# Kernel optimization log

Measured on AMD Instinct MI355X. Metric: run time of the kernel, lower is better.

Reference implementation:

```python
import jax, jax.numpy as jnp
import numpy as np

N, B, E, D, DQ, H = 20000, 32, 320000, 128, 1024, 2
L = N // B  # 625 nodes per graph (equal-size graphs -> static max_node_num)
NUM_GNN_LAYERS = 3


def setup_inputs() -> dict:
    key = jax.random.key(0)
    ks = jax.random.split(key, 32)
    rn = lambda k, s, scale=1.0: jax.random.normal(k, s, jnp.float32) * scale
    w = lambda k, fi, fo: rn(k, (fi, fo), 1.0 / np.sqrt(fi))
    inp = {
        'x': rn(ks[0], (N, D)),
        'edge_attr': rn(ks[1], (E, D)),
        'u': rn(ks[2], (B, D)),
        'qa_attr': rn(ks[3], (B, DQ)),
        # edge MLP: cat(src,dest,edge_attr,u[eb]) = 4D -> hidden D -> D
        'W_e1': w(ks[4], 4 * D, D), 'b_e1': jnp.zeros((D,)),
        'W_e2': w(ks[5], D, D), 'b_e2': jnp.zeros((D,)),
        # weight mlp: cat(edge_attr, u[eb]) = 2D -> 1 (num_layers=1)
        'W_w': w(ks[6], 2 * D, 1), 'b_w': jnp.zeros((1,)),
        # message mlp: cat(x[row], edge_attr) = 2D -> D -> D
        'W_m1': w(ks[7], 2 * D, D), 'b_m1': jnp.zeros((D,)),
        'W_m2': w(ks[8], D, D), 'b_m2': jnp.zeros((D,)),
        # update mlp: cat(x, received, u[nb]) = 3D -> D -> D
        'W_u1': w(ks[9], 3 * D, D), 'b_u1': jnp.zeros((D,)),
        'W_u2': w(ks[10], D, D), 'b_u2': jnp.zeros((D,)),
        # multihead att-pool: q from qa_attr (DQ) -> H*dk; k,v from evidence (D) -> H*dk
        'W_q': w(ks[11], DQ, D), 'b_q': jnp.zeros((D,)),
        'W_k': w(ks[12], D, D), 'b_k': jnp.zeros((D,)),
        'W_v': w(ks[13], D, D), 'b_v': jnp.zeros((D,)),
        'edge_index': jax.random.randint(ks[14], (2, E), 0, N, dtype=jnp.int32),
        'node_batch': (jnp.arange(N, dtype=jnp.int32) // L).astype(jnp.int32),
        'num_of_nodes': jnp.full((B,), L, dtype=jnp.int32),
    }
    return inp


def _mlp2(h, W1, b1, W2, b2):
    return jax.nn.relu(h @ W1 + b1) @ W2 + b2


def _seg_softmax(logits, seg, num):
    m = jax.ops.segment_max(logits, seg, num_segments=num)
    e = jnp.exp(logits - m[seg])
    s = jax.ops.segment_sum(e, seg, num_segments=num)
    return e / s[seg]


def reference(x, edge_attr, u, qa_attr,
              W_e1, b_e1, W_e2, b_e2, W_w, b_w,
              W_m1, b_m1, W_m2, b_m2, W_u1, b_u1, W_u2, b_u2,
              W_q, b_q, W_k, b_k, W_v, b_v,
              edge_index, node_batch, num_of_nodes):
    row, col = edge_index[0], edge_index[1]
    edge_batch = node_batch[row]
    Bsz, Nn = u.shape[0], x.shape[0]
    Lm = Nn // Bsz  # static max_node_num (equal-size graphs)

    norm_w = None
    for _ in range(NUM_GNN_LAYERS):
        ue = u[edge_batch]  # [E, D]
        # EdgeModel: cat(src, dest, edge_attr, u[eb]) -> MLP -> new edge_attr
        new_edge = _mlp2(jnp.concatenate([x[row], x[col], edge_attr, ue], 1),
                         W_e1, b_e1, W_e2, b_e2)
        # edge weights from OLD edge_attr (per EdgeV1Model.forward)
        wts = jnp.concatenate([edge_attr, ue], 1) @ W_w + b_w  # [E,1]
        norm_w = _seg_softmax(wts[:, 0], edge_batch, Bsz)[:, None]  # [E,1]
        edge_attr = new_edge
        # NodeModel: message MLP, weighted scatter_mean over col, update MLP
        msg = _mlp2(jnp.concatenate([x[row], edge_attr], 1), W_m1, b_m1, W_m2, b_m2)
        summed = jax.ops.segment_sum(msg * norm_w, col, num_segments=Nn)
        cnt = jax.ops.segment_sum(jnp.ones((msg.shape[0],), msg.dtype), col, num_segments=Nn)
        received = summed / jnp.maximum(cnt, 1.0)[:, None]
        x = _mlp2(jnp.concatenate([x, received, u[node_batch]], 1),
                  W_u1, b_u1, W_u2, b_u2)

    pooled_edge = jax.ops.segment_sum(edge_attr * norm_w, edge_batch, num_segments=Bsz)  # [B,D]
    # evidence packing: equal graphs -> simple reshape, then exact GELU
    evidence = jax.nn.gelu(x.reshape(Bsz, Lm, -1), approximate=False)  # [B,L,D]
    mask = jnp.arange(Lm)[None, :] >= num_of_nodes[:, None]  # [B,L] True = masked

    # MultiheadAttPoolLayer
    dk = W_k.shape[1] // H
    q = (qa_attr @ W_q + b_q).reshape(Bsz, H, dk)
    k = (evidence @ W_k + b_k).reshape(Bsz, Lm, H, dk)
    v = (evidence @ W_v + b_v).reshape(Bsz, Lm, H, dk)
    scores = jnp.einsum('bhd,blhd->bhl', q, k) / jnp.sqrt(jnp.float32(dk))
    scores = jnp.where(mask[:, None, :], -1e30, scores)
    attn = jax.nn.softmax(scores, axis=-1)
    pooled_node = jnp.einsum('bhl,blhd->bhd', attn, v).reshape(Bsz, H * dk)  # [B,D]

    return jnp.concatenate([pooled_edge, pooled_node], 1)  # [B, 2D]
```

## Files before the change

kernel.cpp:

```cpp
#include <hip/hip_runtime.h>
#include <math.h>

typedef __bf16 bf16_t;
typedef bf16_t bf16x8 __attribute__((ext_vector_type(8)));
typedef bf16_t bf16x4 __attribute__((ext_vector_type(4)));
typedef bf16_t bf16x2 __attribute__((ext_vector_type(2)));
typedef float  f32x4  __attribute__((ext_vector_type(4)));

#define N_NODES 20000
#define NEDGE   320000
#define DIM     128
#define TP      136
#define EBLK    2500
#define FWAVES  10000
#define NBLK    625
#define GPRE    157
#define PBLK    512

#define FE1  0
#define FE2  49152
#define FM1  65536
#define FM2  98304
#define FU1  114688
#define FU2  163840
#define FK   180224
#define FV   196608
#define FWC  212992
#define WF_ELEMS 229376

__device__ __forceinline__ void acc_zero32(f32x4 acc[2][8]) {
  f32x4 z = {0.f, 0.f, 0.f, 0.f};
#pragma unroll
  for (int i = 0; i < 2; ++i)
#pragma unroll
    for (int j = 0; j < 8; ++j) acc[i][j] = z;
}

__device__ __forceinline__ void wstage_rows_bf(bf16_t* sA, const bf16_t* src, int rowreg, int lane) {
  int r = lane >> 1, h = lane & 1;
  int row = __shfl(rowreg, r);
  const bf16_t* sp = src + (size_t)row * DIM + h * 64;
  bf16_t* dp = sA + r * TP + h * 64;
#pragma unroll
  for (int i = 0; i < 8; ++i)
    *(uint4*)(dp + i * 8) = *(const uint4*)(sp + i * 8);
}

__device__ __forceinline__ void wstage_rows_f32(bf16_t* sA, const float* src, int rowreg, int lane) {
  int r = lane >> 1, h = lane & 1;
  int row = __shfl(rowreg, r);
  const float* sp = src + (size_t)row * DIM + h * 64;
  bf16_t* dp = sA + r * TP + h * 64;
#pragma unroll
  for (int i = 0; i < 8; ++i) {
    float4 f0 = *(const float4*)(sp + i * 8);
    float4 f1 = *(const float4*)(sp + i * 8 + 4);
    bf16x8 tv;
    tv[0]=(bf16_t)f0.x; tv[1]=(bf16_t)f0.y; tv[2]=(bf16_t)f0.z; tv[3]=(bf16_t)f0.w;
    tv[4]=(bf16_t)f1.x; tv[5]=(bf16_t)f1.y; tv[6]=(bf16_t)f1.z; tv[7]=(bf16_t)f1.w;
    *(bf16x8*)(dp + i * 8) = tv;
  }
}

__device__ __forceinline__ void wstage_seq_bf(bf16_t* sA, const bf16_t* src, int base, int lane) {
  int r = lane >> 1, h = lane & 1;
  const bf16_t* sp = src + (size_t)(base + r) * DIM + h * 64;
  bf16_t* dp = sA + r * TP + h * 64;
#pragma unroll
  for (int i = 0; i < 8; ++i)
    *(uint4*)(dp + i * 8) = *(const uint4*)(sp + i * 8);
}

__device__ __forceinline__ void wstage_seq_f32(bf16_t* sA, const float* src, int base, int lane) {
  int r = lane >> 1, h = lane & 1;
  const float* sp = src + (size_t)(base + r) * DIM + h * 64;
  bf16_t* dp = sA + r * TP + h * 64;
#pragma unroll
  for (int i = 0; i < 8; ++i) {
    float4 f0 = *(const float4*)(sp + i * 8);
    float4 f1 = *(const float4*)(sp + i * 8 + 4);
    bf16x8 tv;
    tv[0]=(bf16_t)f0.x; tv[1]=(bf16_t)f0.y; tv[2]=(bf16_t)f0.z; tv[3]=(bf16_t)f0.w;
    tv[4]=(bf16_t)f1.x; tv[5]=(bf16_t)f1.y; tv[6]=(bf16_t)f1.z; tv[7]=(bf16_t)f1.w;
    *(bf16x8*)(dp + i * 8) = tv;
  }
}

__device__ __forceinline__ void chunk_stage(bf16_t* ch, const bf16_t* __restrict__ src, int t) {
#pragma unroll
  for (int i = 0; i < 8; ++i) {
    int idx = (i * 256 + t) * 8;
    *(uint4*)(ch + idx) = *(const uint4*)(src + idx);
  }
}

__device__ __forceinline__ void wmfma_lds(const bf16_t* sA, const bf16_t* ch,
                                          int lane, int lm, int lq, f32x4 acc[2][8]) {
#pragma unroll
  for (int kk = 0; kk < 4; ++kk) {
    int ko = kk * 32 + lq * 8;
    bf16x8 a0 = *(const bf16x8*)(sA + lm * TP + ko);
    bf16x8 a1 = *(const bf16x8*)(sA + (16 + lm) * TP + ko);
    const bf16_t* wp = ch + (kk << 12) + (lane << 3);
#pragma unroll
    for (int ct = 0; ct < 8; ++ct) {
      bf16x8 bfr = *(const bf16x8*)(wp + (ct << 9));
      acc[0][ct] = __builtin_amdgcn_mfma_f32_16x16x32_bf16(a0, bfr, acc[0][ct], 0, 0, 0);
      acc[1][ct] = __builtin_amdgcn_mfma_f32_16x16x32_bf16(a1, bfr, acc[1][ct], 0, 0, 0);
    }
  }
}

__device__ __forceinline__ void wmfma_gk128(const bf16_t* sA, const bf16_t* __restrict__ Wf,
                                            int lane, int lm, int lq, f32x4 acc[2][8]) {
#pragma unroll
  for (int kk = 0; kk < 4; ++kk) {
    int ko = kk * 32 + lq * 8;
    bf16x8 a0 = *(const bf16x8*)(sA + lm * TP + ko);
    bf16x8 a1 = *(const bf16x8*)(sA + (16 + lm) * TP + ko);
    const bf16_t* wp = Wf + ((kk * 8) << 9) + (lane << 3);
#pragma unroll
    for (int ct = 0; ct < 8; ++ct) {
      bf16x8 bfr = *(const bf16x8*)(wp + (ct << 9));
      acc[0][ct] = __builtin_amdgcn_mfma_f32_16x16x32_bf16(a0, bfr, acc[0][ct], 0, 0, 0);
      acc[1][ct] = __builtin_amdgcn_mfma_f32_16x16x32_bf16(a1, bfr, acc[1][ct], 0, 0, 0);
    }
  }
}

__device__ __forceinline__ void merge_shfl(float& m, float& s, int width) {
  for (int k = 1; k < width; k <<= 1) {
    float m2 = __shfl_xor(m, k), s2 = __shfl_xor(s, k);
    float M = fmaxf(m, m2), ns = 0.f;
    if (m  > -1e29f) ns += s  * expf(m  - M);
    if (m2 > -1e29f) ns += s2 * expf(m2 - M);
    m = M; s = ns;
  }
}

__global__ void gn_xcvt(const float* x, bf16_t* xb) {
  int i = blockIdx.x * 256 + threadIdx.x;
  if (i < N_NODES * DIM / 4) {
    float4 f = ((const float4*)x)[i];
    bf16x4 o; o[0]=(bf16_t)f.x; o[1]=(bf16_t)f.y; o[2]=(bf16_t)f.z; o[3]=(bf16_t)f.w;
    *(bf16x4*)(xb + (size_t)i * 4) = o;
  }
}

__global__ void gn_wcomb(const float* Wm2, const float* Wu1, float* wc) {
  int idx = blockIdx.x * 256 + threadIdx.x;
  if (idx >= 16384) return;
  int i = idx >> 7, j = idx & 127;
  float acc = 0.f;
  for (int m = 0; m < 128; ++m)
    acc += Wm2[i * 128 + m] * Wu1[(128 + m) * 128 + j];
  wc[idx] = acc;
}

__global__ void gn_fragw(const float* We1, const float* We2, const float* Wm1, const float* Wm2,
                         const float* Wu1, const float* Wu2, const float* Wk, const float* Wv,
                         const float* Wc, bf16_t* WF) {
  int idx = blockIdx.x * 256 + threadIdx.x;
  if (idx >= WF_ELEMS) return;
  int seg = idx >> 14;
  const float* W; int kc;
  switch (seg) {
    case 0:  W = We1; kc = 0; break;
    case 1:  W = We1; kc = 1; break;
    case 2:  W = We1; kc = 2; break;
    case 3:  W = We2; kc = 0; break;
    case 4:  W = Wm1; kc = 0; break;
    case 5:  W = Wm1; kc = 1; break;
    case 6:  W = Wm2; kc = 0; break;
    case 7:  W = Wu1; kc = 0; break;
    case 8:  W = Wu1; kc = 1; break;
    case 9:  W = Wu1; kc = 2; break;
    case 10: W = Wu2; kc = 0; break;
    case 11: W = Wk;  kc = 0; break;
    case 12: W = Wv;  kc = 0; break;
    default: W = Wc;  kc = 0; break;
  }
  int r = idx & 16383;
  int j = r & 7, lane = (r >> 3) & 63, ct = (r >> 9) & 7, kk = (r >> 12) & 3;
  int k = kc * 128 + kk * 32 + (lane >> 4) * 8 + j;
  int n = ct * 16 + (lane & 15);
  WF[idx] = (bf16_t)W[k * 128 + n];
}

__global__ void gn_uprep(const float* u, const float* We1, const float* be1,
                         const float* Ww, const float* bw,
                         const float* bm2, const float* Wu1,
                         float* Rp, float* uw, float* bm2u) {
  int t = threadIdx.x;
  for (int idx = blockIdx.x * 256 + t; idx < 32 * 128; idx += gridDim.x * 256) {
    int g = idx >> 7, c = idx & 127;
    float acc = be1[c];
    for (int k = 0; k < 128; ++k) acc += u[g * 128 + k] * We1[(384 + k) * 128 + c];
    Rp[g * 128 + (c & 15) * 8 + (c >> 4)] = acc;
  }
  if (blockIdx.x == 0 && t < 32) {
    float acc = bw[0];
    for (int k = 0; k < 128; ++k) acc += u[t * 128 + k] * Ww[128 + k];
    uw[t] = acc;
  }
  if (blockIdx.x == 1 && t < 128) {
    float acc = 0.f;
    for (int k = 0; k < 128; ++k) acc += bm2[k] * Wu1[(128 + k) * 128 + t];
    bm2u[t] = acc;
  }
}

__global__ void gn_counti(const int* ei, int* cnti) {
  int e = blockIdx.x * 256 + threadIdx.x;
  if (e < NEDGE) atomicAdd(&cnti[ei[NEDGE + e]], 1);
}

__global__ void gn_scan(const int* cnti, int* off, int* curs) {
  __shared__ int part[256];
  int t = threadIdx.x;
  int base = t * 80;
  int lim = base + 80; if (lim > N_NODES) lim = N_NODES;
  int s = 0;
  for (int i = base; i < lim; ++i) s += cnti[i];
  part[t] = s;
  __syncthreads();
  for (int d = 1; d < 256; d <<= 1) {
    int add = (t >= d) ? part[t - d] : 0;
    __syncthreads();
    part[t] += add;
    __syncthreads();
  }
  int pfx = (t == 0) ? 0 : part[t - 1];
  for (int i = base; i < lim; ++i) {
    off[i] = pfx; curs[i] = pfx; pfx += cnti[i];
  }
  if (t == 0) off[N_NODES] = NEDGE;
}

__global__ void gn_eidx(const int* ei, int* curs, int* eidx) {
  int e = blockIdx.x * 256 + threadIdx.x;
  if (e < NEDGE) {
    int c = ei[NEDGE + e];
    int pos = atomicAdd(&curs[c], 1);
    eidx[pos] = e;
  }
}

__global__ void gn_q(const float* qa, const float* Wq, const float* bq, float* qb) {
  int b = blockIdx.x, t = threadIdx.x;
  int c = t & 127, half = t >> 7;
  const float* qrow = qa + b * 1024 + half * 512;
  float acc = 0.f;
  for (int k = 0; k < 512; ++k) acc += qrow[k] * Wq[(half * 512 + k) * 128 + c];
  __shared__ float red[256];
  red[t] = acc;
  __syncthreads();
  if (half == 0) qb[b * 128 + c] = red[c] + red[128 + c] + bq[c];
}

__global__ void gn_wl0(const float* ea, const float* Ww, const float* uw,
                       const int* ei, const int* nbat, float* wl, int* gb) {
  int t = threadIdx.x;
  int sub = t & 15, grp = t >> 4;
  for (int e = blockIdx.x * 16 + grp; e < NEDGE; e += gridDim.x * 16) {
    const float* er = ea + (size_t)e * DIM + sub * 8;
    float s = 0.f;
#pragma unroll
    for (int j = 0; j < 8; ++j) s += er[j] * Ww[sub * 8 + j];
#pragma unroll
    for (int m = 1; m < 16; m <<= 1) s += __shfl_xor(s, m);
    if (sub == 0) {
      int g = nbat[ei[e]];
      wl[e] = s + uw[g];
      gb[e] = g;
    }
  }
}

__global__ void gn_part0(const float* wl, const int* gb, float* pm, float* ps) {
  __shared__ float lv[128];
  __shared__ int   lgg[128];
  int t = threadIdx.x, blk = blockIdx.x, e0 = blk * 128;
  if (t < 128) { lv[t] = wl[e0 + t]; lgg[t] = gb[e0 + t]; }
  __syncthreads();
  int g = t >> 3, seg = t & 7;
  float m = -1e30f, s = 0.f;
  for (int i = seg * 16; i < seg * 16 + 16; ++i)
    if (lgg[i] == g) {
      float v = lv[i];
      if (v > m) { s = s * expf(m - v) + 1.f; m = v; }
      else s += expf(v - m);
    }
  merge_shfl(m, s, 8);
  if (seg == 0) { pm[g * FWAVES + blk] = m; ps[g * FWAVES + blk] = s; }
}

__global__ void gn_reduce_ms(const float* pm, const float* ps, float* mg, float* sg, int nb) {
  int g = blockIdx.x, t = threadIdx.x;
  __shared__ float red[256];
  float m = -1e30f;
  for (int i = t; i < nb; i += 256) m = fmaxf(m, pm[g * FWAVES + i]);
  red[t] = m; __syncthreads();
  for (int s2 = 128; s2 > 0; s2 >>= 1) { if (t < s2) red[t] = fmaxf(red[t], red[t + s2]); __syncthreads(); }
  m = red[0]; __syncthreads();
  float s = 0.f;
  for (int i = t; i < nb; i += 256) {
    float sb = ps[g * FWAVES + i];
    if (sb > 0.f) s += sb * expf(pm[g * FWAVES + i] - m);
  }
  red[t] = s; __syncthreads();
  for (int s2 = 128; s2 > 0; s2 >>= 1) { if (t < s2) red[t] += red[t + s2]; __syncthreads(); }
  if (t == 0) { mg[g] = m; sg[g] = red[0]; }
}

__global__ __launch_bounds__(256, 2) void gn_fused(
    const bf16_t* __restrict__ xb,
    const void* esrcv, int efirst,
    bf16_t* edst,
    const bf16_t* __restrict__ WF,
    const float* Rp, const float* UW, const float* Wwv,
    const float* be2, const float* bm1,
    const float* wl_cur, const float* mg, const float* sg,
    float* wl_next, float* pm, float* ps, int last,
    const int* ei, const int* gb, bf16_t* msg,
    const float* uu, const float* bu1, const int* nbat, float* pre,
    float* nwout) {
  __shared__ bf16_t chunk[16384];
  __shared__ bf16_t band[4][32 * TP];
  __shared__ float slwt[128];

  int t = threadIdx.x;
  int w = t >> 6, lane = t & 63;
  int lm = lane & 15, lq = lane >> 4;
  int blk = blockIdx.x;
  bf16_t* myband = band[w];

  if (blk >= EBLK) {
    int nb128 = blk - EBLK;
    int gb32 = nb128 * 4 + w;
    int lrow = 0, lgr = 0;
    if (lane < 32) {
      int node = gb32 * 32 + lane;
      if (node > N_NODES - 1) node = N_NODES - 1;
      lrow = node;
      lgr = nbat[node];
    }
    f32x4 acc[2][8];
    acc_zero32(acc);
    wstage_rows_bf(myband, xb, lrow, lane);
    chunk_stage(chunk, WF + FU1, t);
    __syncthreads();
    wmfma_lds(myband, chunk, lane, lm, lq, acc);
    __syncthreads();
    wstage_rows_f32(myband, uu, lgr, lane);
    chunk_stage(chunk, WF + FU1 + 32768, t);
    __syncthreads();
    wmfma_lds(myband, chunk, lane, lm, lq, acc);
    if (gb32 < NBLK) {
      float* pp = pre + (size_t)gb32 * 4096 + lane;
#pragma unroll
      for (int rt = 0; rt < 2; ++rt)
#pragma unroll
        for (int reg = 0; reg < 4; ++reg)
#pragma unroll
          for (int ct = 0; ct < 8; ++ct)
            pp[((rt * 32 + reg * 8 + ct) << 6)] = acc[rt][ct][reg] + bu1[ct * 16 + lm];
    }
    return;
  }

  int e0 = blk * 128;
  int ew0 = e0 + w * 32;
  int lrowr = 0, lcolr = 0, lgr = 0;
  float lnwr = 0.f;
  if (lane < 32) {
    int e = ew0 + lane;
    lrowr = ei[e];
    lcolr = ei[NEDGE + e];
    lgr = gb[e];
    lnwr = expf(wl_cur[e] - mg[lgr]) / sg[lgr];
    nwout[e] = lnwr;
  }

  f32x4 accE[2][8], accM[2][8];
  acc_zero32(accE);
  acc_zero32(accM);

  uint4 c0, c1, c2, c3, c4, c5, c6, c7;
#define CLOAD(SRC) { const uint4* _s = (const uint4*)(SRC) + t; \
  c0 = _s[0];    c1 = _s[256];  c2 = _s[512];  c3 = _s[768]; \
  c4 = _s[1024]; c5 = _s[1280]; c6 = _s[1536]; c7 = _s[1792]; }
#define CWRITE() { uint4* _d = (uint4*)chunk + t; \
  _d[0] = c0;    _d[256] = c1;  _d[512] = c2;  _d[768] = c3; \
  _d[1024] = c4; _d[1280] = c5; _d[1536] = c6; _d[1792] = c7; }

  CLOAD(WF + FE1);
  wstage_rows_bf(myband, xb, lrowr, lane);
  CWRITE();
  __syncthreads();

  CLOAD(WF + FM1);
  wmfma_lds(myband, chunk, lane, lm, lq, accE);
  __syncthreads();
  CWRITE();
  __syncthreads();

  CLOAD(WF + FE1 + 16384);
  wmfma_lds(myband, chunk, lane, lm, lq, accM);
  wstage_rows_bf(myband, xb, lcolr, lane);
  __syncthreads();
  CWRITE();
  __syncthreads();

  CLOAD(WF + FE1 + 32768);
  wmfma_lds(myband, chunk, lane, lm, lq, accE);
  if (efirst) wstage_seq_f32(myband, (const float*)esrcv, ew0, lane);
  else        wstage_seq_bf (myband, (const bf16_t*)esrcv, ew0, lane);
  __syncthreads();
  CWRITE();
  __syncthreads();

  CLOAD(WF + FE2);
  wmfma_lds(myband, chunk, lane, lm, lq, accE);
#pragma unroll
  for (int rt = 0; rt < 2; ++rt)
#pragma unroll
    for (int reg = 0; reg < 4; ++reg) {
      int row = rt * 16 + lq * 4 + reg;
      int g = __shfl(lgr, row);
      const float4* rp = (const float4*)(Rp + (size_t)g * 128 + lm * 8);
      float4 ra = rp[0], rb = rp[1];
      float rv[8] = {ra.x, ra.y, ra.z, ra.w, rb.x, rb.y, rb.z, rb.w};
#pragma unroll
      for (int ct = 0; ct < 8; ++ct) {
        int col = ct * 16 + lm;
        myband[row * TP + col] = (bf16_t)fmaxf(accE[rt][ct][reg] + rv[ct], 0.f);
      }
    }
  acc_zero32(accE);
  __syncthreads();
  CWRITE();
  __syncthreads();

  CLOAD(WF + FM1 + 16384);
  wmfma_lds(myband, chunk, lane, lm, lq, accE);
  {
    float ww8[8], be8[8];
#pragma unroll
    for (int ct = 0; ct < 8; ++ct) { ww8[ct] = Wwv[ct * 16 + lm]; be8[ct] = be2[ct * 16 + lm]; }
#pragma unroll
    for (int rt = 0; rt < 2; ++rt)
#pragma unroll
      for (int reg = 0; reg < 4; ++reg) {
        int row = rt * 16 + lq * 4 + reg;
        int g = __shfl(lgr, row);
        float lsum = 0.f;
#pragma unroll
        for (int ct = 0; ct < 8; ++ct) {
          int col = ct * 16 + lm;
          float v = accE[rt][ct][reg] + be8[ct];
          myband[row * TP + col] = (bf16_t)v;
          lsum += v * ww8[ct];
        }
        if (!last) {
          lsum += __shfl_xor(lsum, 1);
          lsum += __shfl_xor(lsum, 2);
          lsum += __shfl_xor(lsum, 4);
          lsum += __shfl_xor(lsum, 8);
          if (lm == 0) {
            float v2 = lsum + UW[g];
            wl_next[ew0 + row] = v2;
            slwt[w * 32 + row] = v2;
          }
        }
      }
    int r = lane >> 1, h = lane & 1;
    bf16_t* dp = edst + (size_t)(ew0 + r) * DIM + h * 64;
    const bf16_t* sp2 = myband + r * TP + h * 64;
#pragma unroll
    for (int i = 0; i < 8; ++i)
      *(uint4*)(dp + i * 8) = *(const uint4*)(sp2 + i * 8);
  }
  __syncthreads();
  CWRITE();
  __syncthreads();

  wmfma_lds(myband, chunk, lane, lm, lq, accM);
  {
    float bm18[8];
#pragma unroll
    for (int ct = 0; ct < 8; ++ct) bm18[ct] = bm1[ct * 16 + lm];
#pragma unroll
    for (int rt = 0; rt < 2; ++rt)
#pragma unroll
      for (int reg = 0; reg < 4; ++reg) {
        int row = rt * 16 + lq * 4 + reg;
        float nwv = __shfl(lnwr, row);
#pragma unroll
        for (int ct = 0; ct < 8; ++ct) {
          int col = ct * 16 + lm;
          myband[row * TP + col] = (bf16_t)(fmaxf(accM[rt][ct][reg] + bm18[ct], 0.f) * nwv);
        }
      }
    int r = lane >> 1, h = lane & 1;
    bf16_t* dp = msg + (size_t)(ew0 + r) * DIM + h * 64;
    const bf16_t* sp2 = myband + r * TP + h * 64;
#pragma unroll
    for (int i = 0; i < 8; ++i)
      *(uint4*)(dp + i * 8) = *(const uint4*)(sp2 + i * 8);
  }

  if (!last) {
    int g = lane >> 1, seg = lane & 1;
    float m = -1e30f, s = 0.f;
    for (int i = seg * 16; i < seg * 16 + 16; ++i) {
      int gi = __shfl(lgr, i);
      if (gi == g) {
        float v = slwt[w * 32 + i];
        if (v > m) { s = s * expf(m - v) + 1.f; m = v; }
        else s += expf(v - m);
      }
    }
    merge_shfl(m, s, 2);
    if (seg == 0) { pm[g * FWAVES + blk * 4 + w] = m; ps[g * FWAVES + blk * 4 + w] = s; }
  }
#undef CLOAD
#undef CWRITE
}

__global__ __launch_bounds__(256) void gn_gather(
    const bf16_t* __restrict__ msg, const float* __restrict__ nw,
    const int* __restrict__ off, const int* __restrict__ eidx,
    bf16_t* recvb, float* rnw) {
  int w = threadIdx.x >> 6, lane = threadIdx.x & 63;
  int n = blockIdx.x * 4 + w;
  int o0 = off[n], o1 = off[n + 1];
  float a0 = 0.f, a1 = 0.f, snw = 0.f;
  int i = o0;
  int e = (i < o1) ? eidx[i] : 0;
  for (; i < o1; ++i) {
    int en = (i + 1 < o1) ? eidx[i + 1] : 0;
    bf16x2 v = *(const bf16x2*)(msg + (size_t)e * DIM + lane * 2);
    a0 += (float)v[0];
    a1 += (float)v[1];
    snw += nw[e];
    e = en;
  }
  float ic = 1.f / fmaxf((float)(o1 - o0), 1.f);
  bf16x2 o; o[0] = (bf16_t)(a0 * ic); o[1] = (bf16_t)(a1 * ic);
  *(bf16x2*)(recvb + (size_t)n * DIM + lane * 2) = o;
  if (lane == 0) rnw[n] = snw * ic;
}

__global__ __launch_bounds__(64, 3) void gn_node(
    bf16_t* xdst, const bf16_t* recvb, const float* rnw, const float* pre,
    const bf16_t* __restrict__ WF, const float* bu2, const float* bm2u) {
  __shared__ bf16_t sA[32 * TP];

  int lane = threadIdx.x;
  int nb = blockIdx.x;
  int n0 = nb * 32;
  int lm = lane & 15, lq = lane >> 4;

  float rnwreg = 0.f;
  if (lane < 32) rnwreg = rnw[n0 + lane];

  wstage_seq_bf(sA, recvb, n0, lane);

  f32x4 acc[2][8];
  acc_zero32(acc);
  wmfma_gk128(sA, WF + FWC, lane, lm, lq, acc);

  const float* pp = pre + (size_t)nb * 4096 + lane;
  float bm2u8[8];
#pragma unroll
  for (int ct = 0; ct < 8; ++ct) bm2u8[ct] = bm2u[ct * 16 + lm];
#pragma unroll
  for (int rt = 0; rt < 2; ++rt)
#pragma unroll
    for (int reg = 0; reg < 4; ++reg) {
      int row = rt * 16 + lq * 4 + reg;
      float rv = __shfl(rnwreg, row);
#pragma unroll
      for (int ct = 0; ct < 8; ++ct) {
        int col = ct * 16 + lm;
        sA[row * TP + col] = (bf16_t)fmaxf(
            acc[rt][ct][reg] + rv * bm2u8[ct] + pp[((rt * 32 + reg * 8 + ct) << 6)], 0.f);
      }
    }
  acc_zero32(acc);
  wmfma_gk128(sA, WF + FU2, lane, lm, lq, acc);

  {
    float bu28[8];
#pragma unroll
    for (int ct = 0; ct < 8; ++ct) bu28[ct] = bu2[ct * 16 + lm];
#pragma unroll
    for (int rt = 0; rt < 2; ++rt)
#pragma unroll
      for (int reg = 0; reg < 4; ++reg) {
        int row = rt * 16 + lq * 4 + reg;
        bf16_t* dr = xdst + (size_t)(n0 + row) * DIM;
#pragma unroll
        for (int ct = 0; ct < 8; ++ct) {
          int col = ct * 16 + lm;
          dr[col] = (bf16_t)(acc[rt][ct][reg] + bu28[ct]);
        }
      }
  }
}

__global__ __launch_bounds__(64, 3) void gn_ev(
    const bf16_t* xsrc, const bf16_t* __restrict__ WF,
    const float* bk, const float* bv, float* kb, float* vb) {
  __shared__ bf16_t sA[32 * TP];

  int lane = threadIdx.x;
  int n0 = blockIdx.x * 32;
  int sel = blockIdx.y;
  const bf16_t* Wf = WF + (sel ? FV : FK);
  const float* bias = sel ? bv : bk;
  float* dst = sel ? vb : kb;
  int lm = lane & 15, lq = lane >> 4;

  {
    int r = lane >> 1, h = lane & 1;
    const bf16_t* sp = xsrc + (size_t)(n0 + r) * DIM + h * 64;
    bf16_t* dp = sA + r * TP + h * 64;
#pragma unroll
    for (int i = 0; i < 8; ++i) {
      uint4 v = *(const uint4*)(sp + i * 8);
      bf16_t tmp[8];
      *(uint4*)tmp = v;
      bf16x8 tv;
#pragma unroll
      for (int j = 0; j < 8; ++j) {
        float f = (float)tmp[j];
        tv[j] = (bf16_t)(0.5f * f * (1.f + erff(f * 0.70710678118654752f)));
      }
      *(bf16x8*)(dp + i * 8) = tv;
    }
  }

  f32x4 acc[2][8];
  acc_zero32(acc);
  wmfma_gk128(sA, Wf, lane, lm, lq, acc);

  {
    float b8[8];
#pragma unroll
    for (int ct = 0; ct < 8; ++ct) b8[ct] = bias[ct * 16 + lm];
#pragma unroll
    for (int rt = 0; rt < 2; ++rt)
#pragma unroll
      for (int reg = 0; reg < 4; ++reg) {
        int row = rt * 16 + lq * 4 + reg;
        float* dr = dst + (size_t)(n0 + row) * DIM;
#pragma unroll
        for (int ct = 0; ct < 8; ++ct) {
          int col = ct * 16 + lm;
          dr[col] = acc[rt][ct][reg] + b8[ct];
        }
      }
  }
}

__global__ __launch_bounds__(256, 2) void gn_pooled_edge(
    const bf16_t* __restrict__ eb, const float* __restrict__ nw,
    const int* __restrict__ gb, float* pep) {
  __shared__ float loc[4][4096];
  int t = threadIdx.x;
  int lane = t & 63, w = t >> 6;
  float* myloc = loc[w];
  for (int i = lane; i < 4096; i += 64) myloc[i] = 0.f;

  int wid = blockIdx.x * 4 + w;
  int c0 = lane * 2;
  for (int e = wid; e < NEDGE; e += PBLK * 4) {
    int g = gb[e];
    float nwt = nw[e];
    bf16x2 v = *(const bf16x2*)(eb + (size_t)e * DIM + c0);
    float* a = myloc + g * 128 + c0;
    float2 cur = *(float2*)a;
    cur.x += (float)v[0] * nwt;
    cur.y += (float)v[1] * nwt;
    *(float2*)a = cur;
  }
  __syncthreads();
  float* pp = pep + (size_t)blockIdx.x * 4096;
  for (int i = t; i < 4096; i += 256)
    pp[i] = loc[0][i] + loc[1][i] + loc[2][i] + loc[3][i];
}

__global__ void gn_att(const float* qb, const float* kb, const float* vb, const int* non, float* out) {
  int b = blockIdx.x >> 1, h = blockIdx.x & 1, t = threadIdx.x;
  __shared__ float qv[64];
  __shared__ float sc[625];
  __shared__ float red[256];
  if (t < 64) qv[t] = qb[b * 128 + h * 64 + t];
  __syncthreads();
  int nn = non[b];
  const float4* qv4 = (const float4*)qv;
  for (int l = t; l < 625; l += 256) {
    float acc = 0.f;
    const float4* kr = (const float4*)(kb + ((size_t)(b * 625 + l)) * DIM + h * 64);
#pragma unroll
    for (int d2 = 0; d2 < 16; ++d2) {
      float4 kv = kr[d2];
      float4 qq = qv4[d2];
      acc += qq.x * kv.x + qq.y * kv.y + qq.z * kv.z + qq.w * kv.w;
    }
    sc[l] = (l < nn) ? acc * 0.125f : -1e30f;
  }
  __syncthreads();
  float m = -1e30f;
  for (int l = t; l < 625; l += 256) m = fmaxf(m, sc[l]);
  red[t] = m; __syncthreads();
  for (int s2 = 128; s2 > 0; s2 >>= 1) { if (t < s2) red[t] = fmaxf(red[t], red[t + s2]); __syncthreads(); }
  m = red[0]; __syncthreads();
  float ssum = 0.f;
  for (int l = t; l < 625; l += 256) { float e = expf(sc[l] - m); sc[l] = e; ssum += e; }
  red[t] = ssum; __syncthreads();
  for (int s2 = 128; s2 > 0; s2 >>= 1) { if (t < s2) red[t] += red[t + s2]; __syncthreads(); }
  float inv = 1.f / red[0];
  __syncthreads();
  int d = t & 63, seg = t >> 6;
  float acc = 0.f;
  for (int l = seg; l < 625; l += 4) acc += sc[l] * vb[((size_t)(b * 625 + l)) * DIM + h * 64 + d];
  red[t] = acc; __syncthreads();
  if (t < 64) {
    float v = red[t] + red[64 + t] + red[128 + t] + red[192 + t];
    out[b * 256 + 128 + h * 64 + d] = v * inv;
  }
}

__global__ void gn_fin(const float* pep, float* out) {
  int i = blockIdx.x * 256 + threadIdx.x;
  float s = 0.f;
#pragma unroll 8
  for (int blk = 0; blk < PBLK; ++blk) s += pep[(size_t)blk * 4096 + i];
  int b = i >> 7, c = i & 127;
  out[b * 256 + c] = s;
}

extern "C" void kernel_launch(void* const* d_in, const int* in_sizes, int n_in,
                              void* d_out, int out_size, void* d_ws, size_t ws_size,
                              hipStream_t stream) {
  const float* x   = (const float*)d_in[0];
  const float* ea  = (const float*)d_in[1];
  const float* u   = (const float*)d_in[2];
  const float* qa  = (const float*)d_in[3];
  const float* We1 = (const float*)d_in[4];
  const float* be1 = (const float*)d_in[5];
  const float* We2 = (const float*)d_in[6];
  const float* be2 = (const float*)d_in[7];
  const float* Ww  = (const float*)d_in[8];
  const float* bw  = (const float*)d_in[9];
  const float* Wm1 = (const float*)d_in[10];
  const float* bm1 = (const float*)d_in[11];
  const float* Wm2 = (const float*)d_in[12];
  const float* bm2 = (const float*)d_in[13];
  const float* Wu1 = (const float*)d_in[14];
  const float* bu1 = (const float*)d_in[15];
  const float* Wu2 = (const float*)d_in[16];
  const float* bu2 = (const float*)d_in[17];
  const float* Wq  = (const float*)d_in[18];
  const float* bq  = (const float*)d_in[19];
  const float* Wk  = (const float*)d_in[20];
  const float* bk  = (const float*)d_in[21];
  const float* Wv  = (const float*)d_in[22];
  const float* bv  = (const float*)d_in[23];
  const int* ei   = (const int*)d_in[24];
  const int* nbat = (const int*)d_in[25];
  const int* non  = (const int*)d_in[26];
  float* out = (float*)d_out;

  char* p = (char*)d_ws;
  auto alloc = [&](size_t bytes) { char* r = p; p += (bytes + 255) & ~(size_t)255; return r; };
  bf16_t* EB    = (bf16_t*)alloc((size_t)NEDGE * DIM * 2);
  bf16_t* XB    = (bf16_t*)alloc((size_t)N_NODES * DIM * 2);
  bf16_t* XB0   = (bf16_t*)alloc((size_t)N_NODES * DIM * 2);
  bf16_t* MSG   = (bf16_t*)alloc((size_t)NEDGE * DIM * 2);
  bf16_t* RECVB = (bf16_t*)alloc((size_t)N_NODES * DIM * 2);
  int*   CNTI = (int*)alloc((size_t)N_NODES * 4);
  int*   OFF  = (int*)alloc((size_t)(N_NODES + 1) * 4);
  int*   CURS = (int*)alloc((size_t)N_NODES * 4);
  int*   EIDX = (int*)alloc((size_t)NEDGE * 4);
  float* WL   = (float*)alloc((size_t)NEDGE * 4);
  float* WLn  = (float*)alloc((size_t)NEDGE * 4);
  float* NW   = (float*)alloc((size_t)NEDGE * 4);
  float* RNW  = (float*)alloc((size_t)N_NODES * 4);
  int*   GB   = (int*)alloc((size_t)NEDGE * 4);
  float* PM   = (float*)alloc((size_t)32 * FWAVES * 4);
  float* PS   = (float*)alloc((size_t)32 * FWAVES * 4);
  float* MG   = (float*)alloc(32 * 4);
  float* SG   = (float*)alloc(32 * 4);
  float* RP   = (float*)alloc(32 * 128 * 4);
  float* UW   = (float*)alloc(32 * 4);
  float* WCOMB= (float*)alloc(16384 * 4);
  float* BM2U = (float*)alloc(128 * 4);
  bf16_t* WF  = (bf16_t*)alloc((size_t)WF_ELEMS * 2);
  float* QB   = (float*)alloc(32 * 128 * 4);
  float* KB   = (float*)alloc((size_t)N_NODES * DIM * 4);
  float* VB   = (float*)alloc((size_t)N_NODES * DIM * 4);
  float* PEP  = (float*)alloc((size_t)PBLK * 4096 * 4);
  float* PRE  = (float*)alloc((size_t)N_NODES * DIM * 4);

  hipMemsetAsync(CNTI, 0, (size_t)N_NODES * 4, stream);

  gn_xcvt<<<(N_NODES * DIM / 4 + 255) / 256, 256, 0, stream>>>(x, XB0);
  gn_wcomb<<<64, 256, 0, stream>>>(Wm2, Wu1, WCOMB);
  gn_fragw<<<(WF_ELEMS + 255) / 256, 256, 0, stream>>>(We1, We2, Wm1, Wm2, Wu1, Wu2, Wk, Wv, WCOMB, WF);
  gn_uprep<<<16, 256, 0, stream>>>(u, We1, be1, Ww, bw, bm2, Wu1, RP, UW, BM2U);
  gn_counti<<<1250, 256, 0, stream>>>(ei, CNTI);
  gn_scan<<<1, 256, 0, stream>>>(CNTI, OFF, CURS);
  gn_eidx<<<1250, 256, 0, stream>>>(ei, CURS, EIDX);
  gn_q<<<32, 256, 0, stream>>>(qa, Wq, bq, QB);
  gn_wl0<<<2500, 256, 0, stream>>>(ea, Ww, UW, ei, nbat, WL, GB);
  gn_part0<<<EBLK, 256, 0, stream>>>(WL, GB, PM, PS);

  for (int layer = 0; layer < 3; ++layer) {
    int first = (layer == 0) ? 1 : 0;
    int last = (layer == 2) ? 1 : 0;
    const bf16_t* xs = first ? XB0 : XB;
    const void* es = first ? (const void*)ea : (const void*)EB;
    float* cur = (layer == 1) ? WLn : WL;
    float* nxt = (layer == 1) ? WL : WLn;
    gn_reduce_ms<<<32, 256, 0, stream>>>(PM, PS, MG, SG, first ? EBLK : FWAVES);
    gn_fused<<<EBLK + GPRE, 256, 0, stream>>>(xs, es, first, EB, WF, RP, UW, Ww,
                                              be2, bm1, cur, MG, SG,
                                              nxt, PM, PS, last, ei, GB, MSG,
                                              u, bu1, nbat, PRE, NW);
    gn_gather<<<5000, 256, 0, stream>>>(MSG, NW, OFF, EIDX, RECVB, RNW);
    gn_node<<<NBLK, 64, 0, stream>>>(XB, RECVB, RNW, PRE, WF, bu2, BM2U);
  }

  gn_pooled_edge<<<PBLK, 256, 0, stream>>>(EB, NW, GB, PEP);
  gn_ev<<<dim3(NBLK, 2), 64, 0, stream>>>(XB, WF, bk, bv, KB, VB);
  gn_att<<<64, 256, 0, stream>>>(QB, KB, VB, non, out);
  gn_fin<<<16, 256, 0, stream>>>(PEP, out);
}
```

Baseline: 1.320 ms.

## Fold edge second layer into downstream weights, store pre-projection edge hidden state

The edge MLP's second linear layer (We2) is composed algebraically into its consumers: We1's edge-attr slice, Wm1's edge slice, and the weight-logit vector. Each fused edge block therefore runs one fewer 128x128 MFMA stage and stores the ReLU hidden state instead of the projected edge_attr. The pooled-edge output now applies We2 and a per-graph bias term after the weighted segment sum, which needs an extra small kernel. The gather loop is unrolled by four for more memory-level parallelism, and attention pooling uses 1024 threads per block. Composing weights in bf16 changes rounding slightly.

```diff
diff --git a/kernel.cpp b/kernel.cpp
--- a/kernel.cpp
+++ b/kernel.cpp
@@ -18,9 +18,9 @@
 #define PBLK    512
 
 #define FE1  0
-#define FE2  49152
+#define FCE  49152
 #define FM1  65536
-#define FM2  98304
+#define FCM  81920
 #define FU1  114688
 #define FU2  163840
 #define FK   180224
@@ -147,19 +147,28 @@
   }
 }
 
-__global__ void gn_wcomb(const float* Wm2, const float* Wu1, float* wc) {
+__global__ void gn_wcomb(const float* Wm2, const float* Wu1, const float* We2,
+                         const float* We1, const float* Wm1,
+                         float* wc1, float* wce, float* wcm) {
   int idx = blockIdx.x * 256 + threadIdx.x;
   if (idx >= 16384) return;
   int i = idx >> 7, j = idx & 127;
   float acc = 0.f;
-  for (int m = 0; m < 128; ++m)
-    acc += Wm2[i * 128 + m] * Wu1[(128 + m) * 128 + j];
-  wc[idx] = acc;
-}
-
-__global__ void gn_fragw(const float* We1, const float* We2, const float* Wm1, const float* Wm2,
-                         const float* Wu1, const float* Wu2, const float* Wk, const float* Wv,
-                         const float* Wc, bf16_t* WF) {
+  if (blockIdx.y == 0) {
+    for (int m = 0; m < 128; ++m) acc += Wm2[i * 128 + m] * Wu1[(128 + m) * 128 + j];
+    wc1[idx] = acc;
+  } else if (blockIdx.y == 1) {
+    for (int m = 0; m < 128; ++m) acc += We2[i * 128 + m] * We1[(256 + m) * 128 + j];
+    wce[idx] = acc;
+  } else {
+    for (int m = 0; m < 128; ++m) acc += We2[i * 128 + m] * Wm1[(128 + m) * 128 + j];
+    wcm[idx] = acc;
+  }
+}
+
+__global__ void gn_fragw(const float* We1, const float* Wce, const float* Wm1, const float* Wcm,
+                         const float* Wm2, const float* Wu1, const float* Wu2,
+                         const float* Wk, const float* Wv, const float* Wc1, bf16_t* WF) {
   int idx = blockIdx.x * 256 + threadIdx.x;
   if (idx >= WF_ELEMS) return;
   int seg = idx >> 14;
@@ -168,9 +177,9 @@
     case 0:  W = We1; kc = 0; break;
     case 1:  W = We1; kc = 1; break;
     case 2:  W = We1; kc = 2; break;
-    case 3:  W = We2; kc = 0; break;
+    case 3:  W = Wce; kc = 0; break;
     case 4:  W = Wm1; kc = 0; break;
-    case 5:  W = Wm1; kc = 1; break;
+    case 5:  W = Wcm; kc = 0; break;
     case 6:  W = Wm2; kc = 0; break;
     case 7:  W = Wu1; kc = 0; break;
     case 8:  W = Wu1; kc = 1; break;
@@ -178,7 +187,7 @@
     case 10: W = Wu2; kc = 0; break;
     case 11: W = Wk;  kc = 0; break;
     case 12: W = Wv;  kc = 0; break;
-    default: W = Wc;  kc = 0; break;
+    default: W = Wc1; kc = 0; break;
   }
   int r = idx & 16383;
   int j = r & 7, lane = (r >> 3) & 63, ct = (r >> 9) & 7, kk = (r >> 12) & 3;
@@ -190,23 +199,39 @@
 __global__ void gn_uprep(const float* u, const float* We1, const float* be1,
                          const float* Ww, const float* bw,
                          const float* bm2, const float* Wu1,
-                         float* Rp, float* uw, float* bm2u) {
+                         const float* bm1, const float* be2,
+                         const float* Wm1, const float* We2,
+                         float* Rp0, float* Rp12, float* uw, float* uw2,
+                         float* bm2u, float* bm1p, float* wv) {
   int t = threadIdx.x;
   for (int idx = blockIdx.x * 256 + t; idx < 32 * 128; idx += gridDim.x * 256) {
     int g = idx >> 7, c = idx & 127;
     float acc = be1[c];
     for (int k = 0; k < 128; ++k) acc += u[g * 128 + k] * We1[(384 + k) * 128 + c];
-    Rp[g * 128 + (c & 15) * 8 + (c >> 4)] = acc;
+    float be12 = 0.f;
+    for (int k = 0; k < 128; ++k) be12 += be2[k] * We1[(256 + k) * 128 + c];
+    int tc = g * 128 + (c & 15) * 8 + (c >> 4);
+    Rp0[tc] = acc;
+    Rp12[tc] = acc + be12;
   }
   if (blockIdx.x == 0 && t < 32) {
     float acc = bw[0];
     for (int k = 0; k < 128; ++k) acc += u[t * 128 + k] * Ww[128 + k];
+    float bsh = 0.f;
+    for (int c = 0; c < 128; ++c) bsh += be2[c] * Ww[c];
     uw[t] = acc;
+    uw2[t] = acc + bsh;
   }
   if (blockIdx.x == 1 && t < 128) {
-    float acc = 0.f;
-    for (int k = 0; k < 128; ++k) acc += bm2[k] * Wu1[(128 + k) * 128 + t];
-    bm2u[t] = acc;
+    float a1 = 0.f, a2 = 0.f, a3 = 0.f;
+    for (int k = 0; k < 128; ++k) {
+      a1 += bm2[k] * Wu1[(128 + k) * 128 + t];
+      a2 += be2[k] * Wm1[(128 + k) * 128 + t];
+      a3 += We2[t * 128 + k] * Ww[k];
+    }
+    bm2u[t] = a1;
+    bm1p[t] = bm1[t] + a2;
+    wv[t] = a3;
   }
 }
 
@@ -318,8 +343,7 @@
     const void* esrcv, int efirst,
     bf16_t* edst,
     const bf16_t* __restrict__ WF,
-    const float* Rp, const float* UW, const float* Wwv,
-    const float* be2, const float* bm1,
+    const float* Rp, const float* UW2, const float* wv, const float* bm1p,
     const float* wl_cur, const float* mg, const float* sg,
     float* wl_next, float* pm, float* ps, int last,
     const int* ei, const int* gb, bf16_t* msg,
@@ -412,7 +436,7 @@
   CWRITE();
   __syncthreads();
 
-  CLOAD(WF + FE1 + 32768);
+  CLOAD(efirst ? (WF + FE1 + 32768) : (WF + FCE));
   wmfma_lds(myband, chunk, lane, lm, lq, accE);
   if (efirst) wstage_seq_f32(myband, (const float*)esrcv, ew0, lane);
   else        wstage_seq_bf (myband, (const bf16_t*)esrcv, ew0, lane);
@@ -420,45 +444,26 @@
   CWRITE();
   __syncthreads();
 
-  CLOAD(WF + FE2);
-  wmfma_lds(myband, chunk, lane, lm, lq, accE);
-#pragma unroll
-  for (int rt = 0; rt < 2; ++rt)
-#pragma unroll
-    for (int reg = 0; reg < 4; ++reg) {
-      int row = rt * 16 + lq * 4 + reg;
-      int g = __shfl(lgr, row);
-      const float4* rp = (const float4*)(Rp + (size_t)g * 128 + lm * 8);
-      float4 ra = rp[0], rb = rp[1];
-      float rv[8] = {ra.x, ra.y, ra.z, ra.w, rb.x, rb.y, rb.z, rb.w};
-#pragma unroll
-      for (int ct = 0; ct < 8; ++ct) {
-        int col = ct * 16 + lm;
-        myband[row * TP + col] = (bf16_t)fmaxf(accE[rt][ct][reg] + rv[ct], 0.f);
-      }
-    }
-  acc_zero32(accE);
-  __syncthreads();
-  CWRITE();
-  __syncthreads();
-
-  CLOAD(WF + FM1 + 16384);
+  CLOAD(WF + FCM);
   wmfma_lds(myband, chunk, lane, lm, lq, accE);
   {
-    float ww8[8], be8[8];
-#pragma unroll
-    for (int ct = 0; ct < 8; ++ct) { ww8[ct] = Wwv[ct * 16 + lm]; be8[ct] = be2[ct * 16 + lm]; }
+    float ww8[8];
+#pragma unroll
+    for (int ct = 0; ct < 8; ++ct) ww8[ct] = wv[ct * 16 + lm];
 #pragma unroll
     for (int rt = 0; rt < 2; ++rt)
 #pragma unroll
       for (int reg = 0; reg < 4; ++reg) {
         int row = rt * 16 + lq * 4 + reg;
         int g = __shfl(lgr, row);
+        const float4* rp = (const float4*)(Rp + (size_t)g * 128 + lm * 8);
+        float4 ra = rp[0], rb = rp[1];
+        float rv[8] = {ra.x, ra.y, ra.z, ra.w, rb.x, rb.y, rb.z, rb.w};
         float lsum = 0.f;
 #pragma unroll
         for (int ct = 0; ct < 8; ++ct) {
           int col = ct * 16 + lm;
-          float v = accE[rt][ct][reg] + be8[ct];
+          float v = fmaxf(accE[rt][ct][reg] + rv[ct], 0.f);
           myband[row * TP + col] = (bf16_t)v;
           lsum += v * ww8[ct];
         }
@@ -468,7 +473,7 @@
           lsum += __shfl_xor(lsum, 4);
           lsum += __shfl_xor(lsum, 8);
           if (lm == 0) {
-            float v2 = lsum + UW[g];
+            float v2 = lsum + UW2[g];
             wl_next[ew0 + row] = v2;
             slwt[w * 32 + row] = v2;
           }
@@ -489,7 +494,7 @@
   {
     float bm18[8];
 #pragma unroll
-    for (int ct = 0; ct < 8; ++ct) bm18[ct] = bm1[ct * 16 + lm];
+    for (int ct = 0; ct < 8; ++ct) bm18[ct] = bm1p[ct * 16 + lm];
 #pragma unroll
     for (int rt = 0; rt < 2; ++rt)
 #pragma unroll
@@ -537,14 +542,22 @@
   int o0 = off[n], o1 = off[n + 1];
   float a0 = 0.f, a1 = 0.f, snw = 0.f;
   int i = o0;
-  int e = (i < o1) ? eidx[i] : 0;
+  for (; i + 3 < o1; i += 4) {
+    int e0 = eidx[i], e1 = eidx[i + 1], e2 = eidx[i + 2], e3 = eidx[i + 3];
+    bf16x2 v0 = *(const bf16x2*)(msg + (size_t)e0 * DIM + lane * 2);
+    bf16x2 v1 = *(const bf16x2*)(msg + (size_t)e1 * DIM + lane * 2);
+    bf16x2 v2 = *(const bf16x2*)(msg + (size_t)e2 * DIM + lane * 2);
+    bf16x2 v3 = *(const bf16x2*)(msg + (size_t)e3 * DIM + lane * 2);
+    a0 += (float)v0[0] + (float)v1[0] + (float)v2[0] + (float)v3[0];
+    a1 += (float)v0[1] + (float)v1[1] + (float)v2[1] + (float)v3[1];
+    snw += nw[e0] + nw[e1] + nw[e2] + nw[e3];
+  }
   for (; i < o1; ++i) {
-    int en = (i + 1 < o1) ? eidx[i + 1] : 0;
+    int e = eidx[i];
     bf16x2 v = *(const bf16x2*)(msg + (size_t)e * DIM + lane * 2);
     a0 += (float)v[0];
     a1 += (float)v[1];
     snw += nw[e];
-    e = en;
   }
   float ic = 1.f / fmaxf((float)(o1 - o0), 1.f);
   bf16x2 o; o[0] = (bf16_t)(a0 * ic); o[1] = (bf16_t)(a1 * ic);
@@ -666,42 +679,48 @@
 }
 
 __global__ __launch_bounds__(256, 2) void gn_pooled_edge(
-    const bf16_t* __restrict__ eb, const float* __restrict__ nw,
-    const int* __restrict__ gb, float* pep) {
+    const bf16_t* __restrict__ he, const float* __restrict__ nw,
+    const int* __restrict__ gb, float* pep, float* pepn) {
   __shared__ float loc[4][4096];
+  __shared__ float nws[4][32];
   int t = threadIdx.x;
   int lane = t & 63, w = t >> 6;
   float* myloc = loc[w];
   for (int i = lane; i < 4096; i += 64) myloc[i] = 0.f;
+  if (lane < 32) nws[w][lane] = 0.f;
 
   int wid = blockIdx.x * 4 + w;
   int c0 = lane * 2;
   for (int e = wid; e < NEDGE; e += PBLK * 4) {
     int g = gb[e];
     float nwt = nw[e];
-    bf16x2 v = *(const bf16x2*)(eb + (size_t)e * DIM + c0);
+    bf16x2 v = *(const bf16x2*)(he + (size_t)e * DIM + c0);
     float* a = myloc + g * 128 + c0;
     float2 cur = *(float2*)a;
     cur.x += (float)v[0] * nwt;
     cur.y += (float)v[1] * nwt;
     *(float2*)a = cur;
+    if (lane == 0) nws[w][g] += nwt;
   }
   __syncthreads();
   float* pp = pep + (size_t)blockIdx.x * 4096;
   for (int i = t; i < 4096; i += 256)
     pp[i] = loc[0][i] + loc[1][i] + loc[2][i] + loc[3][i];
-}
-
-__global__ void gn_att(const float* qb, const float* kb, const float* vb, const int* non, float* out) {
+  if (t < 32)
+    pepn[blockIdx.x * 32 + t] = nws[0][t] + nws[1][t] + nws[2][t] + nws[3][t];
+}
+
+__global__ __launch_bounds__(1024) void gn_att(
+    const float* qb, const float* kb, const float* vb, const int* non, float* out) {
   int b = blockIdx.x >> 1, h = blockIdx.x & 1, t = threadIdx.x;
   __shared__ float qv[64];
   __shared__ float sc[625];
-  __shared__ float red[256];
+  __shared__ float red[1024];
   if (t < 64) qv[t] = qb[b * 128 + h * 64 + t];
   __syncthreads();
   int nn = non[b];
   const float4* qv4 = (const float4*)qv;
-  for (int l = t; l < 625; l += 256) {
+  for (int l = t; l < 625; l += 1024) {
     float acc = 0.f;
     const float4* kr = (const float4*)(kb + ((size_t)(b * 625 + l)) * DIM + h * 64);
 #pragma unroll
@@ -714,33 +733,48 @@
   }
   __syncthreads();
   float m = -1e30f;
-  for (int l = t; l < 625; l += 256) m = fmaxf(m, sc[l]);
+  for (int l = t; l < 625; l += 1024) m = fmaxf(m, sc[l]);
   red[t] = m; __syncthreads();
-  for (int s2 = 128; s2 > 0; s2 >>= 1) { if (t < s2) red[t] = fmaxf(red[t], red[t + s2]); __syncthreads(); }
+  for (int s2 = 512; s2 > 0; s2 >>= 1) { if (t < s2) red[t] = fmaxf(red[t], red[t + s2]); __syncthreads(); }
   m = red[0]; __syncthreads();
   float ssum = 0.f;
-  for (int l = t; l < 625; l += 256) { float e = expf(sc[l] - m); sc[l] = e; ssum += e; }
+  for (int l = t; l < 625; l += 1024) { float e = expf(sc[l] - m); sc[l] = e; ssum += e; }
   red[t] = ssum; __syncthreads();
-  for (int s2 = 128; s2 > 0; s2 >>= 1) { if (t < s2) red[t] += red[t + s2]; __syncthreads(); }
+  for (int s2 = 512; s2 > 0; s2 >>= 1) { if (t < s2) red[t] += red[t + s2]; __syncthreads(); }
   float inv = 1.f / red[0];
   __syncthreads();
   int d = t & 63, seg = t >> 6;
   float acc = 0.f;
-  for (int l = seg; l < 625; l += 4) acc += sc[l] * vb[((size_t)(b * 625 + l)) * DIM + h * 64 + d];
+  for (int l = seg; l < 625; l += 16) acc += sc[l] * vb[((size_t)(b * 625 + l)) * DIM + h * 64 + d];
   red[t] = acc; __syncthreads();
   if (t < 64) {
-    float v = red[t] + red[64 + t] + red[128 + t] + red[192 + t];
+    float v = 0.f;
+#pragma unroll
+    for (int s = 0; s < 16; ++s) v += red[s * 64 + t];
     out[b * 256 + 128 + h * 64 + d] = v * inv;
   }
 }
 
-__global__ void gn_fin(const float* pep, float* out) {
+__global__ void gn_fin1(const float* pep, const float* pepn, float* spool, float* nwg) {
   int i = blockIdx.x * 256 + threadIdx.x;
   float s = 0.f;
 #pragma unroll 8
   for (int blk = 0; blk < PBLK; ++blk) s += pep[(size_t)blk * 4096 + i];
+  spool[i] = s;
+  if (i < 32) {
+    float sn = 0.f;
+    for (int blk = 0; blk < PBLK; ++blk) sn += pepn[blk * 32 + i];
+    nwg[i] = sn;
+  }
+}
+
+__global__ void gn_fin2(const float* spool, const float* nwg, const float* We2,
+                        const float* be2, float* out) {
+  int i = blockIdx.x * 256 + threadIdx.x;
   int b = i >> 7, c = i & 127;
-  out[b * 256 + c] = s;
+  float acc = nwg[b] * be2[c];
+  for (int k = 0; k < 128; ++k) acc += spool[b * 128 + k] * We2[k * 128 + c];
+  out[b * 256 + c] = acc;
 }
 
 extern "C" void kernel_launch(void* const* d_in, const int* in_sizes, int n_in,
@@ -795,23 +829,33 @@
   float* PS   = (float*)alloc((size_t)32 * FWAVES * 4);
   float* MG   = (float*)alloc(32 * 4);
   float* SG   = (float*)alloc(32 * 4);
-  float* RP   = (float*)alloc(32 * 128 * 4);
+  float* RP0  = (float*)alloc(32 * 128 * 4);
+  float* RP12 = (float*)alloc(32 * 128 * 4);
   float* UW   = (float*)alloc(32 * 4);
-  float* WCOMB= (float*)alloc(16384 * 4);
+  float* UW2  = (float*)alloc(32 * 4);
+  float* WC1  = (float*)alloc(16384 * 4);
+  float* WCE  = (float*)alloc(16384 * 4);
+  float* WCM  = (float*)alloc(16384 * 4);
   float* BM2U = (float*)alloc(128 * 4);
+  float* BM1P = (float*)alloc(128 * 4);
+  float* WVV  = (float*)alloc(128 * 4);
   bf16_t* WF  = (bf16_t*)alloc((size_t)WF_ELEMS * 2);
   float* QB   = (float*)alloc(32 * 128 * 4);
   float* KB   = (float*)alloc((size_t)N_NODES * DIM * 4);
   float* VB   = (float*)alloc((size_t)N_NODES * DIM * 4);
   float* PEP  = (float*)alloc((size_t)PBLK * 4096 * 4);
+  float* PEPN = (float*)alloc((size_t)PBLK * 32 * 4);
+  float* SPOOL= (float*)alloc(4096 * 4);
+  float* NWG  = (float*)alloc(32 * 4);
   float* PRE  = (float*)alloc((size_t)N_NODES * DIM * 4);
 
   hipMemsetAsync(CNTI, 0, (size_t)N_NODES * 4, stream);
 
   gn_xcvt<<<(N_NODES * DIM / 4 + 255) / 256, 256, 0, stream>>>(x, XB0);
-  gn_wcomb<<<64, 256, 0, stream>>>(Wm2, Wu1, WCOMB);
-  gn_fragw<<<(WF_ELEMS + 255) / 256, 256, 0, stream>>>(We1, We2, Wm1, Wm2, Wu1, Wu2, Wk, Wv, WCOMB, WF);
-  gn_uprep<<<16, 256, 0, stream>>>(u, We1, be1, Ww, bw, bm2, Wu1, RP, UW, BM2U);
+  gn_wcomb<<<dim3(64, 3), 256, 0, stream>>>(Wm2, Wu1, We2, We1, Wm1, WC1, WCE, WCM);
+  gn_fragw<<<(WF_ELEMS + 255) / 256, 256, 0, stream>>>(We1, WCE, Wm1, WCM, Wm2, Wu1, Wu2, Wk, Wv, WC1, WF);
+  gn_uprep<<<16, 256, 0, stream>>>(u, We1, be1, Ww, bw, bm2, Wu1, bm1, be2, Wm1, We2,
+                                   RP0, RP12, UW, UW2, BM2U, BM1P, WVV);
   gn_counti<<<1250, 256, 0, stream>>>(ei, CNTI);
   gn_scan<<<1, 256, 0, stream>>>(CNTI, OFF, CURS);
   gn_eidx<<<1250, 256, 0, stream>>>(ei, CURS, EIDX);
@@ -824,19 +868,20 @@
     int last = (layer == 2) ? 1 : 0;
     const bf16_t* xs = first ? XB0 : XB;
     const void* es = first ? (const void*)ea : (const void*)EB;
+    const float* rp = first ? RP0 : RP12;
     float* cur = (layer == 1) ? WLn : WL;
     float* nxt = (layer == 1) ? WL : WLn;
     gn_reduce_ms<<<32, 256, 0, stream>>>(PM, PS, MG, SG, first ? EBLK : FWAVES);
-    gn_fused<<<EBLK + GPRE, 256, 0, stream>>>(xs, es, first, EB, WF, RP, UW, Ww,
-                                              be2, bm1, cur, MG, SG,
-                                              nxt, PM, PS, last, ei, GB, MSG,
+    gn_fused<<<EBLK + GPRE, 256, 0, stream>>>(xs, es, first, EB, WF, rp, UW2, WVV, BM1P,
+                                              cur, MG, SG, nxt, PM, PS, last, ei, GB, MSG,
                                               u, bu1, nbat, PRE, NW);
     gn_gather<<<5000, 256, 0, stream>>>(MSG, NW, OFF, EIDX, RECVB, RNW);
     gn_node<<<NBLK, 64, 0, stream>>>(XB, RECVB, RNW, PRE, WF, bu2, BM2U);
   }
 
-  gn_pooled_edge<<<PBLK, 256, 0, stream>>>(EB, NW, GB, PEP);
+  gn_pooled_edge<<<PBLK, 256, 0, stream>>>(EB, NW, GB, PEP, PEPN);
   gn_ev<<<dim3(NBLK, 2), 64, 0, stream>>>(XB, WF, bk, bv, KB, VB);
-  gn_att<<<64, 256, 0, stream>>>(QB, KB, VB, non, out);
-  gn_fin<<<16, 256, 0, stream>>>(PEP, out);
-}
+  gn_att<<<64, 1024, 0, stream>>>(QB, KB, VB, non, out);
+  gn_fin1<<<16, 256, 0, stream>>>(PEP, PEPN, SPOOL, NWG);
+  gn_fin2<<<16, 256, 0, stream>>>(SPOOL, NWG, We2, be2, out);
+}
```

New measurement: 1.259 ms. 4.6% less time.
